# Optimization experiments

Measured on AMD Instinct MI355X. Metric: run time of the kernel, lower is better.

The kernel has to match this reference:

```python
import jax, jax.numpy as jnp
import numpy as np

EPS = 1e-08
TARGET_MARGIN = 1e-3


def setup_inputs() -> dict:
    key = jax.random.key(0)
    k1, k2, k3 = jax.random.split(key, 3)
    B, L, N = 256, 512, 4
    preds = jax.random.normal(k1, (B, L, N), dtype=jnp.float32)
    targets = jax.random.uniform(k2, (B, L, N), dtype=jnp.float32)
    masks = jax.random.randint(k3, (B, L, N), 0, 2).astype(jnp.bool_)
    return {"preds": preds, "targets": targets, "masks": masks}


def _bce_with_logits(x, t):
    # numerically stable binary_cross_entropy_with_logits, reduction='none'
    return jnp.maximum(x, 0.0) - x * t + jax.nn.softplus(-jnp.abs(x))


def reference(preds, targets, masks):
    B, L, N = preds.shape
    # valid ordered pairs: col > row (strict upper triangle over batch)
    pair = jnp.arange(B)[None, :] > jnp.arange(B)[:, None]  # (B, B)

    # scan over the (small) feature axis N to keep peak memory at one
    # (B, B, L) pairwise tensor at a time, matching the chunked original.
    ps = jnp.transpose(preds, (2, 0, 1))    # (N, B, L)
    ts = jnp.transpose(targets, (2, 0, 1))  # (N, B, L)
    ms = jnp.transpose(masks, (2, 0, 1))    # (N, B, L)

    def step(acc, xs):
        p, t, m = xs  # each (B, L)
        x = p[:, None, :] - p[None, :, :]                       # (B, B, L) pred diff
        tg = ((t[:, None, :] - t[None, :, :]) > TARGET_MARGIN).astype(p.dtype)
        mf = jnp.logical_and(jnp.logical_and(m[:, None, :], m[None, :, :]),
                             pair[:, :, None])                  # (B, B, L)
        mfl = mf.astype(p.dtype)
        bce = _bce_with_logits(x, tg)
        loss_sum = jnp.sum(bce * mfl)
        mask_sum = jnp.sum(mfl)
        loss_n = jnp.where(mask_sum > 0, loss_sum / (mask_sum + EPS), 0.0)
        return acc + loss_n, None

    total, _ = jax.lax.scan(step, jnp.zeros((), preds.dtype), (ps, ts, ms))
    return total / N
```

## Files before the change

kernel.cpp:

```cpp
#include <hip/hip_runtime.h>

constexpr int B    = 256;
constexpr int NCOL = 2048;

#define MARGIN 1e-3f
#define LOG2E  1.4426950408889634f
#define LN2    0.6931471805599453

constexpr size_t OFF_SLAB   = 0;
constexpr size_t OFF_CPAIRS = 8192;

__global__ __launch_bounds__(256) void col_pair_kernel(
    const float* __restrict__ preds,
    const float* __restrict__ targets,
    const int*   __restrict__ masks,
    float* __restrict__ slab,
    float* __restrict__ cpairs)
{
    const int col  = blockIdx.x;
    const int t    = threadIdx.x;
    const int lane = t & 63;
    const int wave = t >> 6;

    const int   mv = masks[t * NCOL + col];
    const float uv = preds[t * NCOL + col] * LOG2E;
    const float tv = targets[t * NCOL + col];

    __shared__ float2 sc[256];
    __shared__ int    wcnt[4];
    __shared__ float  s4[4];

    const unsigned long long bal = __ballot(mv != 0);
    if (lane == 0) wcnt[wave] = __popcll(bal);
    __syncthreads();

    int basr = 0;
    #pragma unroll
    for (int w = 0; w < 4; ++w) basr += (w < wave) ? wcnt[w] : 0;
    const int c = wcnt[0] + wcnt[1] + wcnt[2] + wcnt[3];

    if (mv) {
        const int rank = basr + __popcll(bal & ((1ull << lane) - 1ull));
        sc[rank] = make_float2(uv, tv);
    }
    __syncthreads();

    float lg = 0.f, pp = 1.f;
    if (t < c) {
        const float2 av = sc[t];
        for (int d = 1; d < c - t; ++d) {
            const float2 bv = sc[t + d];
            const float x  = av.x - bv.x;
            const float td = av.y - bv.y;
            const float xp = (td > MARGIN) ? -x : x;
            pp *= (__builtin_exp2f(xp) + 1.0f);
            if ((d & 7) == 0) { lg += __builtin_log2f(pp); pp = 1.f; }
        }
    }
    lg += __builtin_log2f(pp);

    #pragma unroll
    for (int off = 32; off > 0; off >>= 1)
        lg += __shfl_down(lg, off, 64);
    if (lane == 0) s4[wave] = lg;
    __syncthreads();

    if (t == 0) {
        slab[col]   = s4[0] + s4[1] + s4[2] + s4[3];
        cpairs[col] = (float)((c * (c - 1)) / 2);
    }
}

__global__ __launch_bounds__(256) void finalize_kernel(
    const float* __restrict__ slab,
    const float* __restrict__ cpairs,
    float* __restrict__ out)
{
    const int t = threadIdx.x;
    double ls = 0.0, cs = 0.0;
    for (int q = t; q < NCOL; q += 256) {
        ls += (double)slab[q];
        cs += (double)cpairs[q];
    }

    __shared__ double sl[256], sp[256], res[4];
    sl[t] = ls; sp[t] = cs;
    __syncthreads();

    if (t < 4) {
        double lsn = 0.0, csn = 0.0;
        for (int g = t; g < 256; g += 4) { lsn += sl[g]; csn += sp[g]; }
        res[t] = (csn > 0.0) ? (LN2 * lsn / (csn + 1e-8)) : 0.0;
    }
    __syncthreads();

    if (t == 0)
        out[0] = (float)((res[0] + res[1] + res[2] + res[3]) * 0.25);
}

extern "C" void kernel_launch(void* const* d_in, const int* in_sizes, int n_in,
                              void* d_out, int out_size, void* d_ws, size_t ws_size,
                              hipStream_t stream)
{
    const float* preds   = (const float*)d_in[0];
    const float* targets = (const float*)d_in[1];
    const int*   masks   = (const int*)d_in[2];
    float* out = (float*)d_out;

    char* ws = (char*)d_ws;
    float* slab   = (float*)(ws + OFF_SLAB);
    float* cpairs = (float*)(ws + OFF_CPAIRS);

    col_pair_kernel<<<NCOL, 256, 0, stream>>>(preds, targets, masks, slab, cpairs);
    finalize_kernel<<<1, 256, 0, stream>>>(slab, cpairs, out);
}
```

Measured before the change: 39.26 us.

## Balance triangular pair loop with circular-offset work split across waves

Replaces the per-thread triangular loop, where thread t handles c-1-t partners, with a circular-distance scheme. Each element pairs with the next K=(c-1)/2 elements modulo c. The distance range is split evenly across the four waves, and the diametric pairs for even c are handled separately. This removes the heavy load imbalance in which low-index threads do most of the work while others sit idle. In exchange the inner loop needs extra wrap logic and the sign flip for wrapped pairs.

```diff
diff --git a/kernel.cpp b/kernel.cpp
--- a/kernel.cpp
+++ b/kernel.cpp
@@ -45,19 +45,51 @@
     }
     __syncthreads();
 
-    float lg = 0.f, pp = 1.f;
-    if (t < c) {
-        const float2 av = sc[t];
-        for (int d = 1; d < c - t; ++d) {
-            const float2 bv = sc[t + d];
-            const float x  = av.x - bv.x;
-            const float td = av.y - bv.y;
-            const float xp = (td > MARGIN) ? -x : x;
-            pp *= (__builtin_exp2f(xp) + 1.0f);
-            if ((d & 7) == 0) { lg += __builtin_log2f(pp); pp = 1.f; }
+    const int K   = (c >= 1) ? ((c - 1) >> 1) : 0;
+    const int dlo = (wave * K) / 4 + 1;
+    const int dhi = ((wave + 1) * K) / 4;
+
+    float lg = 0.f;
+
+    #pragma unroll
+    for (int q = 0; q < 4; ++q) {
+        const int a = lane + 64 * q;
+        if (a < c) {
+            const float2 av = sc[a];
+            float pp = 1.f;
+            for (int d = dlo; d <= dhi; ++d) {
+                int b = a + d;
+                const bool wr = (b >= c);
+                b = wr ? b - c : b;
+                const float2 bv = sc[b];
+                const float x  = av.x - bv.x;
+                const float td = av.y - bv.y;
+                const bool pos = wr ? (td < -MARGIN) : (td > MARGIN);
+                const float xp = (pos != wr) ? -x : x;
+                pp *= (__builtin_exp2f(xp) + 1.0f);
+                if ((d & 7) == 7) { lg += __builtin_log2f(pp); pp = 1.f; }
+            }
+            lg += __builtin_log2f(pp);
         }
     }
-    lg += __builtin_log2f(pp);
+
+    if (wave == 3 && c >= 2 && (c & 1) == 0) {
+        const int hc = c >> 1;
+        float pp = 1.f;
+        #pragma unroll
+        for (int q = 0; q < 2; ++q) {
+            const int a = lane + 64 * q;
+            if (a < hc) {
+                const float2 av = sc[a];
+                const float2 bv = sc[a + hc];
+                const float x  = av.x - bv.x;
+                const float td = av.y - bv.y;
+                const float xp = (td > MARGIN) ? -x : x;
+                pp *= (__builtin_exp2f(xp) + 1.0f);
+            }
+        }
+        lg += __builtin_log2f(pp);
+    }
 
     #pragma unroll
     for (int off = 32; off > 0; off >>= 1)
```

Result: slower. 41.24 us (+5.1%).
